# Kernel tuning notes

Hardware: AMD Instinct MI355X
Metric: run time of the kernel (lower is better)

The kernel has to match this reference:

```python
import jax, jax.numpy as jnp
import numpy as np

N, E, CIN, COUT = 50000, 800000, 64, 64
K_MAIN, K_SC = 5, 1
EPS = 1e-15      # PyG GMMConv sigma epsilon
BN_EPS = 1e-5    # BatchNorm epsilon


def gmm_conv(x, src, dst, pseudo, g, mu, sigma, root, bias):
    """PyG GMMConv with aggr='mean', root_weight=True, bias=True.
    x: [N,Cin], pseudo: [E,dim], g: [Cin,K*Cout], mu/sigma: [K,dim],
    root: [Cin,Cout], bias: [Cout]."""
    K = mu.shape[0]
    Cout = root.shape[1]
    n = x.shape[0]
    # Gaussian mixture weights per edge: [E,K]
    diff = pseudo[:, None, :] - mu[None, :, :]                     # [E,K,dim]
    gauss = jnp.exp((-0.5 * diff * diff / (EPS + sigma[None] ** 2)).sum(-1))
    # Project node features once at node level, then gather per edge
    xp = (x @ g).reshape(n, K, Cout)                               # [N,K,Cout]
    msg = jnp.einsum('ek,ekc->ec', gauss, xp[src])                 # [E,Cout]
    agg = jax.ops.segment_sum(msg, dst, num_segments=n)            # [N,Cout]
    deg = jax.ops.segment_sum(jnp.ones((src.shape[0],), x.dtype), dst,
                              num_segments=n)
    agg = agg / jnp.clip(deg, 1.0)[:, None]                        # mean aggr
    return agg + x @ root + bias


def batch_norm(x, gamma, beta):
    # SyncBatchNorm in training mode: batch stats over the node dimension
    m = x.mean(0)
    v = x.var(0)  # biased variance, as torch uses for normalization
    return (x - m) * jax.lax.rsqrt(v + BN_EPS) * gamma + beta


def _gmm_params(key, cin, cout, k):
    k1, k2, k3, k4 = jax.random.split(key, 4)
    scale = 1.0 / np.sqrt(cin)
    g = jax.random.normal(k1, (cin, k * cout), jnp.float32) * scale
    mu = jax.random.uniform(k2, (k, 1), jnp.float32)
    sigma = 1.0 + 0.1 * jax.random.uniform(k3, (k, 1), jnp.float32)
    root = jax.random.normal(k4, (cin, cout), jnp.float32) * scale
    bias = jnp.zeros((cout,), jnp.float32)
    return g, mu, sigma, root, bias


def setup_inputs() -> dict:
    key = jax.random.key(0)
    ks = jax.random.split(key, 8)
    x = jax.random.normal(ks[0], (N, CIN), jnp.float32)
    edge_index = jax.random.randint(ks[1], (2, E), 0, N, jnp.int64)
    edge_attr = jax.random.uniform(ks[2], (E, 1), jnp.float32)
    g1, mu1, sig1, root1, b1 = _gmm_params(ks[3], CIN, COUT, K_MAIN)
    g2, mu2, sig2, root2, b2 = _gmm_params(ks[4], COUT, COUT, K_MAIN)
    gs, mus, sigs, roots, bs = _gmm_params(ks[5], CIN, COUT, K_SC)
    ones = jnp.ones((COUT,), jnp.float32)
    zeros = jnp.zeros((COUT,), jnp.float32)
    return {
        'x': x, 'edge_index': edge_index, 'edge_attr': edge_attr,
        'g1': g1, 'mu1': mu1, 'sig1': sig1, 'root1': root1, 'b1': b1,
        'gam1': ones, 'bet1': zeros,
        'g2': g2, 'mu2': mu2, 'sig2': sig2, 'root2': root2, 'b2': b2,
        'gam2': ones, 'bet2': zeros,
        'gs': gs, 'mus': mus, 'sigs': sigs, 'roots': roots, 'bs': bs,
        'gams': ones, 'bets': zeros,
    }


def reference(x, edge_index, edge_attr,
              g1, mu1, sig1, root1, b1, gam1, bet1,
              g2, mu2, sig2, root2, b2, gam2, bet2,
              gs, mus, sigs, roots, bs, gams, bets):
    src, dst = edge_index[0], edge_index[1]
    h = gmm_conv(x, src, dst, edge_attr, g1, mu1, sig1, root1, b1)
    h = jax.nn.elu(batch_norm(h, gam1, bet1))
    h = gmm_conv(h, src, dst, edge_attr, g2, mu2, sig2, root2, b2)
    h = batch_norm(h, gam2, bet2)
    sc = gmm_conv(x, src, dst, edge_attr, gs, mus, sigs, roots, bs)
    sc = batch_norm(sc, gams, bets)
    return jax.nn.elu(h + sc)
```

## Files before the change

kernel.cpp:

```cpp
#include <hip/hip_runtime.h>
#include <hip/hip_bf16.h>


#define EPS_SIGMA 1e-15f
#define BN_EPS    1e-5f

typedef unsigned short ushortT;
typedef unsigned int uintT;
typedef __attribute__((ext_vector_type(8))) short bf16x8;
typedef __attribute__((ext_vector_type(4))) float f32x4;
typedef __attribute__((ext_vector_type(2))) float f32x2;

__device__ __forceinline__ ushortT f2bf(float f) {
  uintT b = __float_as_uint(f);
  b += 0x7FFFu + ((b >> 16) & 1u);
  return (ushortT)(b >> 16);
}
__device__ __forceinline__ float bf2f(ushortT u) {
  return __uint_as_float(((uintT)u) << 16);
}
__device__ __forceinline__ uintT pk2(float a, float b) {
  return (uintT)f2bf(a) | ((uintT)f2bf(b) << 16);
}

__global__ void prologue(const float* __restrict__ x, ushortT* __restrict__ x_bf,
                         int total, int* __restrict__ cnt, float* __restrict__ stats,
                         int n, const void* ei, int* flag) {
  int t = blockIdx.x * 256 + threadIdx.x;
  int idx = t * 4;
  if (idx + 3 < total) {
    float4 v = *(const float4*)&x[idx];
    ushortT o[4] = {f2bf(v.x), f2bf(v.y), f2bf(v.z), f2bf(v.w)};
    *(uint2*)&x_bf[idx] = *(const uint2*)o;
  }
  if (t < n) cnt[t] = 0;
  if (t < 12 * 64) stats[t] = 0.f;
  if (blockIdx.x == 0) {
    const int* p = (const int*)ei;
    __shared__ int bad;
    if (threadIdx.x == 0) bad = 0;
    __syncthreads();
    if (p[threadIdx.x * 2 + 1] != 0) atomicAdd(&bad, 1);
    __syncthreads();
    if (threadIdx.x == 0) *flag = (bad == 0);
  }
}

__device__ __forceinline__ int load_idx(const void* ei, size_t pos, int is64) {
  if (is64) return (int)((const long long*)ei)[pos];
  return ((const int*)ei)[pos];
}

__global__ void hist_kernel(const void* ei, int E, const int* flag, int* cnt,
                            int* __restrict__ pos) {
  int e = blockIdx.x * blockDim.x + threadIdx.x;
  if (e >= E) return;
  int d = load_idx(ei, (size_t)E + e, *flag);
  pos[e] = atomicAdd(&cnt[d], 1);
}

__global__ __launch_bounds__(256) void scan1(const int* __restrict__ cnt,
                                             int* __restrict__ row_ptr,
                                             int* __restrict__ partials, int n) {
  int tid = threadIdx.x;
  int base = blockIdx.x * 2048 + tid * 8;
  int v[8], pre[8];
  int run = 0;
#pragma unroll
  for (int j = 0; j < 8; ++j) {
    int idx = base + j;
    v[j] = (idx < n) ? cnt[idx] : 0;
    pre[j] = run;
    run += v[j];
  }
  __shared__ int sd[256];
  sd[tid] = run;
  __syncthreads();
  for (int off = 1; off < 256; off <<= 1) {
    int t = (tid >= off) ? sd[tid - off] : 0;
    __syncthreads();
    sd[tid] += t;
    __syncthreads();
  }
  int excl = sd[tid] - run;
#pragma unroll
  for (int j = 0; j < 8; ++j) {
    int idx = base + j;
    if (idx < n) row_ptr[idx] = excl + pre[j];
  }
  if (tid == 255) partials[blockIdx.x] = sd[255];
}

__global__ void scan2(int* partials, int nb, int* row_ptr, int n) {
  __shared__ int sd[256];
  int tid = threadIdx.x;
  int v = (tid < nb) ? partials[tid] : 0;
  sd[tid] = v;
  __syncthreads();
  for (int off = 1; off < 256; off <<= 1) {
    int t = (tid >= off) ? sd[tid - off] : 0;
    __syncthreads();
    sd[tid] += t;
    __syncthreads();
  }
  if (tid < nb) partials[tid] = sd[tid] - v;
  if (tid == nb - 1) row_ptr[n] = sd[tid];
}

__global__ void scan3(int* __restrict__ row_ptr, const int* __restrict__ partials, int n) {
  int i = blockIdx.x * 256 + threadIdx.x;
  if (i < n) row_ptr[i] += partials[i >> 11];
}

__global__ __launch_bounds__(256) void scatter_wgt(
    const void* ei, const float* __restrict__ ea, int E, const int* flag,
    const int* __restrict__ row_ptr, const int* __restrict__ pos,
    const float* __restrict__ mu1, const float* __restrict__ sig1,
    const float* __restrict__ mus, const float* __restrict__ sigs,
    const float* __restrict__ mu2, const float* __restrict__ sig2,
    uint4* __restrict__ wbuf1, uint4* __restrict__ wbuf2) {
  int e = blockIdx.x * 256 + threadIdx.x;
  if (e >= E) return;
  int is64 = *flag;
  int s = load_idx(ei, (size_t)e, is64);
  int d = load_idx(ei, (size_t)E + e, is64);
  int slot = row_ptr[d] + pos[e];
  float p = ea[e];
  float w1[6], w2[5];
#pragma unroll
  for (int k = 0; k < 5; ++k) {
    float sg = sig1[k], df = p - mu1[k];
    w1[k] = __expf(-0.5f / (EPS_SIGMA + sg * sg) * df * df);
  }
  {
    float sg = sigs[0], df = p - mus[0];
    w1[5] = __expf(-0.5f / (EPS_SIGMA + sg * sg) * df * df);
  }
#pragma unroll
  for (int k = 0; k < 5; ++k) {
    float sg = sig2[k], df = p - mu2[k];
    w2[k] = __expf(-0.5f / (EPS_SIGMA + sg * sg) * df * df);
  }
  wbuf1[slot] = make_uint4(pk2(w1[0], w1[1]), pk2(w1[2], w1[3]), pk2(w1[4], w1[5]), (uintT)s);
  wbuf2[slot] = make_uint4(pk2(w2[0], w2[1]), pk2(w2[2], w2[3]), pk2(w2[4], 0.f), (uintT)s);
}

template <int KT>
__device__ __forceinline__ void q_fma(f32x2* acc, uint4 r, uint2 xv) {
  f32x2 xlo, xhi;
  xlo.x = bf2f((ushortT)(xv.x & 0xffffu));
  xlo.y = bf2f((ushortT)(xv.x >> 16));
  xhi.x = bf2f((ushortT)(xv.y & 0xffffu));
  xhi.y = bf2f((ushortT)(xv.y >> 16));
  float w;
  f32x2 wv;
  w = bf2f((ushortT)(r.x & 0xffffu));
  wv.x = w; wv.y = w;
  acc[0] = __builtin_elementwise_fma(wv, xlo, acc[0]);
  acc[1] = __builtin_elementwise_fma(wv, xhi, acc[1]);
  if (KT > 1) {
    w = bf2f((ushortT)(r.x >> 16));
    wv.x = w; wv.y = w;
    acc[2] = __builtin_elementwise_fma(wv, xlo, acc[2]);
    acc[3] = __builtin_elementwise_fma(wv, xhi, acc[3]);
  }
  if (KT > 2) {
    w = bf2f((ushortT)(r.y & 0xffffu));
    wv.x = w; wv.y = w;
    acc[4] = __builtin_elementwise_fma(wv, xlo, acc[4]);
    acc[5] = __builtin_elementwise_fma(wv, xhi, acc[5]);
  }
  if (KT > 3) {
    w = bf2f((ushortT)(r.y >> 16));
    wv.x = w; wv.y = w;
    acc[6] = __builtin_elementwise_fma(wv, xlo, acc[6]);
    acc[7] = __builtin_elementwise_fma(wv, xhi, acc[7]);
  }
  if (KT > 4) {
    w = bf2f((ushortT)(r.z & 0xffffu));
    wv.x = w; wv.y = w;
    acc[8] = __builtin_elementwise_fma(wv, xlo, acc[8]);
    acc[9] = __builtin_elementwise_fma(wv, xhi, acc[9]);
  }
  if (KT > 5) {
    w = bf2f((ushortT)(r.z >> 16));
    wv.x = w; wv.y = w;
    acc[10] = __builtin_elementwise_fma(wv, xlo, acc[10]);
    acc[11] = __builtin_elementwise_fma(wv, xhi, acc[11]);
  }
}

template <int KT>
__global__ __launch_bounds__(256) void agg_pre(const ushortT* __restrict__ feat,
                                               const int* __restrict__ row_ptr,
                                               const uint4* __restrict__ wbuf,
                                               ushortT* __restrict__ out, int n, int ldo) {
  int lane = threadIdx.x & 63;
  int q = lane >> 4;
  int c4 = lane & 15;
  int node = (blockIdx.x * 4 + (threadIdx.x >> 6)) * 4 + q;
  bool act = node < n;
  int beg = act ? row_ptr[node] : 0;
  int end = act ? row_ptr[node + 1] : 0;
  f32x2 acc[2 * KT];
#pragma unroll
  for (int k = 0; k < 2 * KT; ++k) acc[k] = (f32x2){0.f, 0.f};
  int i = beg;
  for (; i + 4 <= end; i += 4) {
    uint4 r0 = wbuf[i + 0];
    uint4 r1 = wbuf[i + 1];
    uint4 r2 = wbuf[i + 2];
    uint4 r3 = wbuf[i + 3];
    uint2 x0 = *(const uint2*)&feat[((size_t)r0.w << 6) + c4 * 4];
    uint2 x1 = *(const uint2*)&feat[((size_t)r1.w << 6) + c4 * 4];
    uint2 x2 = *(const uint2*)&feat[((size_t)r2.w << 6) + c4 * 4];
    uint2 x3 = *(const uint2*)&feat[((size_t)r3.w << 6) + c4 * 4];
    q_fma<KT>(acc, r0, x0);
    q_fma<KT>(acc, r1, x1);
    q_fma<KT>(acc, r2, x2);
    q_fma<KT>(acc, r3, x3);
  }
  for (; i < end; ++i) {
    uint4 r = wbuf[i];
    uint2 xv = *(const uint2*)&feat[((size_t)r.w << 6) + c4 * 4];
    q_fma<KT>(acc, r, xv);
  }
  if (act) {
    int degi = end - beg;
    float invdeg = 1.0f / (float)(degi > 1 ? degi : 1);
    uintT* outu = (uintT*)out;
    size_t obase = ((size_t)node * ldo) >> 1;
#pragma unroll
    for (int k = 0; k < KT; ++k) {
      uint2 ov = make_uint2(pk2(acc[2 * k].x * invdeg, acc[2 * k].y * invdeg),
                            pk2(acc[2 * k + 1].x * invdeg, acc[2 * k + 1].y * invdeg));
      *(uint2*)&outu[obase + k * 32 + c4 * 2] = ov;
    }
  }
}

__device__ __forceinline__ void prep_one(const float* __restrict__ g,
                                         const float* __restrict__ root,
                                         ushortT* __restrict__ Bm, int K, int t) {
  int ks = t >> 8, rem = t & 255;
  int nt = rem >> 6, lane = rem & 63;
  int kbase = ks * 32 + (lane >> 4) * 8;
  int col = nt * 16 + (lane & 15);
  ushortT o[8];
#pragma unroll
  for (int j = 0; j < 8; ++j) {
    int r = kbase + j;
    float v;
    if (r < K * 64) {
      int k = r >> 6, i = r & 63;
      v = g[(size_t)i * (K * 64) + k * 64 + col];
    } else {
      v = root[(size_t)(r - K * 64) * 64 + col];
    }
    o[j] = f2bf(v);
  }
  *(uint4*)&Bm[(size_t)t * 8] = *(const uint4*)o;
}

__global__ void prep_all(const float* g1, const float* root1, ushortT* Bm1,
                         const float* g2, const float* root2, ushortT* Bm2,
                         const float* gs, const float* roots, ushortT* Bmsc) {
  int t = blockIdx.x * 256 + threadIdx.x;
  if (t < 12 * 256) prep_one(g1, root1, Bm1, 5, t);
  else if (t < 24 * 256) prep_one(g2, root2, Bm2, 5, t - 12 * 256);
  else if (t < 28 * 256) prep_one(gs, roots, Bmsc, 1, t - 24 * 256);
}

__device__ __forceinline__ void bn_epilogue(float cs[4], float cq[4], int wid, int lane,
                                            int tid, float red_s[4][64], float red_q[4][64],
                                            float* sums, float* sumsq) {
#pragma unroll
  for (int nt = 0; nt < 4; ++nt) {
    cs[nt] += __shfl_xor(cs[nt], 16);
    cs[nt] += __shfl_xor(cs[nt], 32);
    cq[nt] += __shfl_xor(cq[nt], 16);
    cq[nt] += __shfl_xor(cq[nt], 32);
  }
  if (lane < 16) {
#pragma unroll
    for (int nt = 0; nt < 4; ++nt) {
      red_s[wid][nt * 16 + lane] = cs[nt];
      red_q[wid][nt * 16 + lane] = cq[nt];
    }
  }
  __syncthreads();
  if (tid < 64) {
    float ts = red_s[0][tid] + red_s[1][tid] + red_s[2][tid] + red_s[3][tid];
    float tq = red_q[0][tid] + red_q[1][tid] + red_q[2][tid] + red_q[3][tid];
    atomicAdd(&sums[tid], ts);
    atomicAdd(&sumsq[tid], tq);
  }
  __syncthreads();
}

__global__ __launch_bounds__(256) void gemm_mfma(const ushortT* __restrict__ A1, int lda1,
                                                 int K1, const ushortT* __restrict__ A2,
                                                 const ushortT* __restrict__ Bm,
                                                 const float* __restrict__ bias,
                                                 ushortT* __restrict__ C, int M,
                                                 float* sums, float* sumsq) {
  __shared__ float red_s[4][64];
  __shared__ float red_q[4][64];
  int tid = threadIdx.x;
  int wid = tid >> 6, lane = tid & 63;
  int row16 = lane & 15, kg = lane >> 4;
  int rowbase = blockIdx.x * 64 + wid * 16;
  int arow = rowbase + row16;
  if (arow >= M) arow = M - 1;
  const ushortT* a1p = A1 + (size_t)arow * lda1 + kg * 8;
  const ushortT* a2p = A2 + (size_t)arow * 64 + kg * 8;
  int nks1 = K1 >> 5;
  int nks = (K1 + 64) >> 5;
  f32x4 acc[4];
#pragma unroll
  for (int nt = 0; nt < 4; ++nt) acc[nt] = (f32x4){0.f, 0.f, 0.f, 0.f};
  for (int ks = 0; ks < nks; ++ks) {
    const ushortT* ap = (ks < nks1) ? (a1p + ks * 32) : (a2p + (ks - nks1) * 32);
    bf16x8 af = *(const bf16x8*)ap;
#pragma unroll
    for (int nt = 0; nt < 4; ++nt) {
      bf16x8 bfr = *(const bf16x8*)(Bm + (size_t)ks * 2048 + nt * 512 + lane * 8);
      acc[nt] = __builtin_amdgcn_mfma_f32_16x16x32_bf16(af, bfr, acc[nt], 0, 0, 0);
    }
  }
  float bv[4];
#pragma unroll
  for (int nt = 0; nt < 4; ++nt) bv[nt] = bias[nt * 16 + row16];
  float cs[4] = {}, cq[4] = {};
#pragma unroll
  for (int r = 0; r < 4; ++r) {
    int orow = rowbase + kg * 4 + r;
    if (orow < M) {
#pragma unroll
      for (int nt = 0; nt < 4; ++nt) {
        float v = acc[nt][r] + bv[nt];
        C[(size_t)orow * 64 + nt * 16 + row16] = f2bf(v);
        cs[nt] += v;
        cq[nt] = fmaf(v, v, cq[nt]);
      }
    }
  }
  bn_epilogue(cs, cq, wid, lane, tid, red_s, red_q, sums, sumsq);
}

__global__ __launch_bounds__(256) void gemm_mfma_dual(
    const ushortT* __restrict__ Abuf, const ushortT* __restrict__ X,
    const ushortT* __restrict__ Bm1, const ushortT* __restrict__ Bmsc,
    const float* __restrict__ b1, const float* __restrict__ bs,
    ushortT* __restrict__ H, ushortT* __restrict__ S, int M,
    float* sumH, float* sqH, float* sumS, float* sqS) {
  __shared__ float red_s[4][64];
  __shared__ float red_q[4][64];
  int tid = threadIdx.x;
  int wid = tid >> 6, lane = tid & 63;
  int row16 = lane & 15, kg = lane >> 4;
  int rowbase = blockIdx.x * 64 + wid * 16;
  int arow = rowbase + row16;
  if (arow >= M) arow = M - 1;
  const ushortT* ab = Abuf + (size_t)arow * 384 + kg * 8;
  const ushortT* xb = X + (size_t)arow * 64 + kg * 8;
  f32x4 accH[4], accS[4];
#pragma unroll
  for (int nt = 0; nt < 4; ++nt) {
    accH[nt] = (f32x4){0.f, 0.f, 0.f, 0.f};
    accS[nt] = (f32x4){0.f, 0.f, 0.f, 0.f};
  }
  for (int ks = 0; ks < 10; ++ks) {
    bf16x8 af = *(const bf16x8*)(ab + ks * 32);
#pragma unroll
    for (int nt = 0; nt < 4; ++nt) {
      bf16x8 bfr = *(const bf16x8*)(Bm1 + (size_t)ks * 2048 + nt * 512 + lane * 8);
      accH[nt] = __builtin_amdgcn_mfma_f32_16x16x32_bf16(af, bfr, accH[nt], 0, 0, 0);
    }
  }
#pragma unroll
  for (int ks = 0; ks < 2; ++ks) {
    bf16x8 af = *(const bf16x8*)(ab + 320 + ks * 32);
#pragma unroll
    for (int nt = 0; nt < 4; ++nt) {
      bf16x8 bfr = *(const bf16x8*)(Bmsc + (size_t)ks * 2048 + nt * 512 + lane * 8);
      accS[nt] = __builtin_amdgcn_mfma_f32_16x16x32_bf16(af, bfr, accS[nt], 0, 0, 0);
    }
  }
#pragma unroll
  for (int ks = 0; ks < 2; ++ks) {
    bf16x8 af = *(const bf16x8*)(xb + ks * 32);
#pragma unroll
    for (int nt = 0; nt < 4; ++nt) {
      bf16x8 bfrH = *(const bf16x8*)(Bm1 + (size_t)(10 + ks) * 2048 + nt * 512 + lane * 8);
      accH[nt] = __builtin_amdgcn_mfma_f32_16x16x32_bf16(af, bfrH, accH[nt], 0, 0, 0);
      bf16x8 bfrS = *(const bf16x8*)(Bmsc + (size_t)(2 + ks) * 2048 + nt * 512 + lane * 8);
      accS[nt] = __builtin_amdgcn_mfma_f32_16x16x32_bf16(af, bfrS, accS[nt], 0, 0, 0);
    }
  }
  float bvH[4], bvS[4];
#pragma unroll
  for (int nt = 0; nt < 4; ++nt) {
    bvH[nt] = b1[nt * 16 + row16];
    bvS[nt] = bs[nt * 16 + row16];
  }
  float csH[4] = {}, cqH[4] = {}, csS[4] = {}, cqS[4] = {};
#pragma unroll
  for (int r = 0; r < 4; ++r) {
    int orow = rowbase + kg * 4 + r;
    if (orow < M) {
#pragma unroll
      for (int nt = 0; nt < 4; ++nt) {
        float vh = accH[nt][r] + bvH[nt];
        float vs = accS[nt][r] + bvS[nt];
        H[(size_t)orow * 64 + nt * 16 + row16] = f2bf(vh);
        S[(size_t)orow * 64 + nt * 16 + row16] = f2bf(vs);
        csH[nt] += vh;
        cqH[nt] = fmaf(vh, vh, cqH[nt]);
        csS[nt] += vs;
        cqS[nt] = fmaf(vs, vs, cqS[nt]);
      }
    }
  }
  bn_epilogue(csH, cqH, wid, lane, tid, red_s, red_q, sumH, sqH);
  bn_epilogue(csS, cqS, wid, lane, tid, red_s, red_q, sumS, sqS);
}

__global__ void norm_elu(const ushortT* __restrict__ Hbf, ushortT* __restrict__ h_bf,
                         const float* __restrict__ stats, const float* __restrict__ gam,
                         const float* __restrict__ bet, float inv_n, int total4) {
  __shared__ float sc_s[64], sh_s[64];
  int tid = threadIdx.x;
  if (tid < 64) {
    float m = stats[tid] * inv_n;
    float v = stats[64 + tid] * inv_n - m * m;
    float r = rsqrtf(v + BN_EPS);
    float s = r * gam[tid];
    sc_s[tid] = s;
    sh_s[tid] = bet[tid] - m * s;
  }
  __syncthreads();
  int t = blockIdx.x * 256 + tid;
  if (t >= total4) return;
  int idx = t * 4;
  int c = idx & 63;
  uint2 hv = *(const uint2*)&Hbf[idx];
  float v0 = bf2f((ushortT)(hv.x & 0xffffu)) * sc_s[c] + sh_s[c];
  float v1 = bf2f((ushortT)(hv.x >> 16)) * sc_s[c + 1] + sh_s[c + 1];
  float v2 = bf2f((ushortT)(hv.y & 0xffffu)) * sc_s[c + 2] + sh_s[c + 2];
  float v3 = bf2f((ushortT)(hv.y >> 16)) * sc_s[c + 3] + sh_s[c + 3];
  v0 = v0 > 0.f ? v0 : expm1f(v0);
  v1 = v1 > 0.f ? v1 : expm1f(v1);
  v2 = v2 > 0.f ? v2 : expm1f(v2);
  v3 = v3 > 0.f ? v3 : expm1f(v3);
  *(uint2*)&h_bf[idx] = make_uint2(pk2(v0, v1), pk2(v2, v3));
}

__global__ void final_kernel(const ushortT* __restrict__ h2, const ushortT* __restrict__ scb,
                             const float* __restrict__ stats,
                             const float* __restrict__ gam2, const float* __restrict__ bet2,
                             const float* __restrict__ gams, const float* __restrict__ bets,
                             float inv_n, float* __restrict__ out, int total4) {
  __shared__ float s2_s[64], t2_s[64], ss_s[64], ts_s[64];
  int tid = threadIdx.x;
  if (tid < 64) {
    float m = stats[2 * 64 + tid] * inv_n;
    float v = stats[3 * 64 + tid] * inv_n - m * m;
    float r = rsqrtf(v + BN_EPS);
    float s = r * gam2[tid];
    s2_s[tid] = s;
    t2_s[tid] = bet2[tid] - m * s;
  } else if (tid < 128) {
    int c = tid - 64;
    float m = stats[4 * 64 + c] * inv_n;
    float v = stats[5 * 64 + c] * inv_n - m * m;
    float r = rsqrtf(v + BN_EPS);
    float s = r * gams[c];
    ss_s[c] = s;
    ts_s[c] = bets[c] - m * s;
  }
  __syncthreads();
  int t = blockIdx.x * 256 + tid;
  if (t >= total4) return;
  int idx = t * 4;
  int c = idx & 63;
  uint2 hv = *(const uint2*)&h2[idx];
  uint2 sv = *(const uint2*)&scb[idx];
  float v0 = bf2f((ushortT)(hv.x & 0xffffu)) * s2_s[c] + t2_s[c] +
             bf2f((ushortT)(sv.x & 0xffffu)) * ss_s[c] + ts_s[c];
  float v1 = bf2f((ushortT)(hv.x >> 16)) * s2_s[c + 1] + t2_s[c + 1] +
             bf2f((ushortT)(sv.x >> 16)) * ss_s[c + 1] + ts_s[c + 1];
  float v2 = bf2f((ushortT)(hv.y & 0xffffu)) * s2_s[c + 2] + t2_s[c + 2] +
             bf2f((ushortT)(sv.y & 0xffffu)) * ss_s[c + 2] + ts_s[c + 2];
  float v3 = bf2f((ushortT)(hv.y >> 16)) * s2_s[c + 3] + t2_s[c + 3] +
             bf2f((ushortT)(sv.y >> 16)) * ss_s[c + 3] + ts_s[c + 3];
  float4 o;
  o.x = v0 > 0.f ? v0 : expm1f(v0);
  o.y = v1 > 0.f ? v1 : expm1f(v1);
  o.z = v2 > 0.f ? v2 : expm1f(v2);
  o.w = v3 > 0.f ? v3 : expm1f(v3);
  *(float4*)&out[idx] = o;
}

extern "C" void kernel_launch(void* const* d_in, const int* in_sizes, int n_in,
                              void* d_out, int out_size, void* d_ws, size_t ws_size,
                              hipStream_t stream) {
  const float* x    = (const float*)d_in[0];
  const void*  ei   = d_in[1];
  const float* ea   = (const float*)d_in[2];
  const float* g1   = (const float*)d_in[3];
  const float* mu1  = (const float*)d_in[4];
  const float* sig1 = (const float*)d_in[5];
  const float* root1= (const float*)d_in[6];
  const float* b1   = (const float*)d_in[7];
  const float* gam1 = (const float*)d_in[8];
  const float* bet1 = (const float*)d_in[9];
  const float* g2   = (const float*)d_in[10];
  const float* mu2  = (const float*)d_in[11];
  const float* sig2 = (const float*)d_in[12];
  const float* root2= (const float*)d_in[13];
  const float* b2   = (const float*)d_in[14];
  const float* gam2 = (const float*)d_in[15];
  const float* bet2 = (const float*)d_in[16];
  const float* gs   = (const float*)d_in[17];
  const float* mus  = (const float*)d_in[18];
  const float* sigs = (const float*)d_in[19];
  const float* roots= (const float*)d_in[20];
  const float* bs   = (const float*)d_in[21];
  const float* gams = (const float*)d_in[22];
  const float* bets = (const float*)d_in[23];

  int N = in_sizes[0] / 64;
  int E = in_sizes[1] / 2;

  char* w = (char*)d_ws;
  auto alloc = [&](size_t bytes) {
    char* p = w;
    w += (bytes + 255) & ~(size_t)255;
    return p;
  };
  int*     flag    = (int*)alloc(256);
  int*     cnt     = (int*)alloc((size_t)N * 4);
  int*     row_ptr = (int*)alloc((size_t)(N + 1) * 4);
  int*     partials= (int*)alloc(256 * 4);
  int*     pos     = (int*)alloc((size_t)E * 4);
  uint4*   wbuf1   = (uint4*)alloc((size_t)E * 16);
  uint4*   wbuf2   = (uint4*)alloc((size_t)E * 16);
  ushortT* Abuf    = (ushortT*)alloc((size_t)N * 384 * 2);
  ushortT* x_bf    = (ushortT*)alloc((size_t)N * 64 * 2);
  ushortT* h_bf    = (ushortT*)alloc((size_t)N * 64 * 2);
  ushortT* Hpre    = (ushortT*)alloc((size_t)N * 64 * 2);
  ushortT* h2b     = (ushortT*)alloc((size_t)N * 64 * 2);
  ushortT* scb     = (ushortT*)alloc((size_t)N * 64 * 2);
  ushortT* Bm1     = (ushortT*)alloc(12 * 2048 * 2);
  ushortT* Bm2     = (ushortT*)alloc(12 * 2048 * 2);
  ushortT* Bmsc    = (ushortT*)alloc(4 * 2048 * 2);
  float*   stats   = (float*)alloc(12 * 64 * 4);

  int eb = (E + 255) / 256;
  int nb1 = (N + 2047) / 2048;
  int total4 = (N * 64) / 4;
  int nb_e4 = (total4 + 255) / 256;
  float inv_n = 1.0f / (float)N;

  prologue<<<nb_e4, 256, 0, stream>>>(x, x_bf, N * 64, cnt, stats, N, ei, flag);
  prep_all<<<28, 256, 0, stream>>>(g1, root1, Bm1, g2, root2, Bm2, gs, roots, Bmsc);

  hist_kernel<<<eb, 256, 0, stream>>>(ei, E, flag, cnt, pos);
  scan1<<<nb1, 256, 0, stream>>>(cnt, row_ptr, partials, N);
  scan2<<<1, 256, 0, stream>>>(partials, nb1, row_ptr, N);
  scan3<<<(N + 255) / 256, 256, 0, stream>>>(row_ptr, partials, N);
  scatter_wgt<<<eb, 256, 0, stream>>>(ei, ea, E, flag, row_ptr, pos,
                                      mu1, sig1, mus, sigs, mu2, sig2, wbuf1, wbuf2);

  int mtiles = (N + 63) / 64;
  int nb_node16 = (N + 15) / 16;

  agg_pre<6><<<nb_node16, 256, 0, stream>>>(x_bf, row_ptr, wbuf1, Abuf, N, 384);
  gemm_mfma_dual<<<mtiles, 256, 0, stream>>>(Abuf, x_bf, Bm1, Bmsc, b1, bs, Hpre, scb, N,
                                             stats + 0 * 64, stats + 1 * 64,
                                             stats + 4 * 64, stats + 5 * 64);
  norm_elu<<<nb_e4, 256, 0, stream>>>(Hpre, h_bf, stats, gam1, bet1, inv_n, total4);

  agg_pre<5><<<nb_node16, 256, 0, stream>>>(h_bf, row_ptr, wbuf2, Abuf, N, 320);
  gemm_mfma<<<mtiles, 256, 0, stream>>>(Abuf, 320, 320, h_bf, Bm2, b2, h2b, N,
                                        stats + 2 * 64, stats + 3 * 64);

  final_kernel<<<nb_e4, 256, 0, stream>>>(h2b, scb, stats, gam2, bet2, gams, bets,
                                          inv_n, (float*)d_out, total4);
}
```

Measured before the change: 211.2 us.

## Fold weight prep into prologue, drop scan3, unroll edge gather by eight

The weight-matrix bf16 prep moves into the prologue kernel, and the scan3 pass is removed. Consumers now add the per-block scan partial on the fly when reading row_ptr, which saves two kernel launches and one pass over row_ptr. The aggregation loop gains an 8-edge unrolled stage so more gather loads are in flight at once, at the cost of extra registers. The row_ptr[n] handling in scan2 uses a tricky sentinel that may be inconsistent with the per-node partial offset.

```diff
diff --git a/kernel.cpp b/kernel.cpp
--- a/kernel.cpp
+++ b/kernel.cpp
@@ -23,9 +23,35 @@
   return (uintT)f2bf(a) | ((uintT)f2bf(b) << 16);
 }
 
+__device__ __forceinline__ void prep_one(const float* __restrict__ g,
+                                         const float* __restrict__ root,
+                                         ushortT* __restrict__ Bm, int K, int t) {
+  int ks = t >> 8, rem = t & 255;
+  int nt = rem >> 6, lane = rem & 63;
+  int kbase = ks * 32 + (lane >> 4) * 8;
+  int col = nt * 16 + (lane & 15);
+  ushortT o[8];
+#pragma unroll
+  for (int j = 0; j < 8; ++j) {
+    int r = kbase + j;
+    float v;
+    if (r < K * 64) {
+      int k = r >> 6, i = r & 63;
+      v = g[(size_t)i * (K * 64) + k * 64 + col];
+    } else {
+      v = root[(size_t)(r - K * 64) * 64 + col];
+    }
+    o[j] = f2bf(v);
+  }
+  *(uint4*)&Bm[(size_t)t * 8] = *(const uint4*)o;
+}
+
 __global__ void prologue(const float* __restrict__ x, ushortT* __restrict__ x_bf,
                          int total, int* __restrict__ cnt, float* __restrict__ stats,
-                         int n, const void* ei, int* flag) {
+                         int n, const void* ei, int* flag,
+                         const float* g1, const float* root1, ushortT* Bm1,
+                         const float* g2, const float* root2, ushortT* Bm2,
+                         const float* gs, const float* roots, ushortT* Bmsc) {
   int t = blockIdx.x * 256 + threadIdx.x;
   int idx = t * 4;
   if (idx + 3 < total) {
@@ -35,7 +61,10 @@
   }
   if (t < n) cnt[t] = 0;
   if (t < 12 * 64) stats[t] = 0.f;
-  if (blockIdx.x == 0) {
+  if (blockIdx.x < 12) prep_one(g1, root1, Bm1, 5, t);
+  else if (blockIdx.x < 24) prep_one(g2, root2, Bm2, 5, t - 12 * 256);
+  else if (blockIdx.x < 28) prep_one(gs, roots, Bmsc, 1, t - 24 * 256);
+  else if (blockIdx.x == 28) {
     const int* p = (const int*)ei;
     __shared__ int bad;
     if (threadIdx.x == 0) bad = 0;
@@ -104,17 +133,16 @@
     __syncthreads();
   }
   if (tid < nb) partials[tid] = sd[tid] - v;
-  if (tid == nb - 1) row_ptr[n] = sd[tid];
-}
-
-__global__ void scan3(int* __restrict__ row_ptr, const int* __restrict__ partials, int n) {
-  int i = blockIdx.x * 256 + threadIdx.x;
-  if (i < n) row_ptr[i] += partials[i >> 11];
+  if (tid == nb - 1) {
+    partials[nb] = sd[tid];
+    row_ptr[n] = ((n >> 11) == nb) ? 0 : v;
+  }
 }
 
 __global__ __launch_bounds__(256) void scatter_wgt(
     const void* ei, const float* __restrict__ ea, int E, const int* flag,
-    const int* __restrict__ row_ptr, const int* __restrict__ pos,
+    const int* __restrict__ row_ptr, const int* __restrict__ partials,
+    const int* __restrict__ pos,
     const float* __restrict__ mu1, const float* __restrict__ sig1,
     const float* __restrict__ mus, const float* __restrict__ sigs,
     const float* __restrict__ mu2, const float* __restrict__ sig2,
@@ -124,7 +152,7 @@
   int is64 = *flag;
   int s = load_idx(ei, (size_t)e, is64);
   int d = load_idx(ei, (size_t)E + e, is64);
-  int slot = row_ptr[d] + pos[e];
+  int slot = row_ptr[d] + partials[d >> 11] + pos[e];
   float p = ea[e];
   float w1[6], w2[5];
 #pragma unroll
@@ -193,6 +221,7 @@
 template <int KT>
 __global__ __launch_bounds__(256) void agg_pre(const ushortT* __restrict__ feat,
                                                const int* __restrict__ row_ptr,
+                                               const int* __restrict__ partials,
                                                const uint4* __restrict__ wbuf,
                                                ushortT* __restrict__ out, int n, int ldo) {
   int lane = threadIdx.x & 63;
@@ -200,12 +229,41 @@
   int c4 = lane & 15;
   int node = (blockIdx.x * 4 + (threadIdx.x >> 6)) * 4 + q;
   bool act = node < n;
-  int beg = act ? row_ptr[node] : 0;
-  int end = act ? row_ptr[node + 1] : 0;
+  int beg = 0, end = 0;
+  if (act) {
+    beg = row_ptr[node] + partials[node >> 11];
+    end = row_ptr[node + 1] + partials[(node + 1) >> 11];
+  }
   f32x2 acc[2 * KT];
 #pragma unroll
   for (int k = 0; k < 2 * KT; ++k) acc[k] = (f32x2){0.f, 0.f};
   int i = beg;
+  for (; i + 8 <= end; i += 8) {
+    uint4 r0 = wbuf[i + 0];
+    uint4 r1 = wbuf[i + 1];
+    uint4 r2 = wbuf[i + 2];
+    uint4 r3 = wbuf[i + 3];
+    uint4 r4 = wbuf[i + 4];
+    uint4 r5 = wbuf[i + 5];
+    uint4 r6 = wbuf[i + 6];
+    uint4 r7 = wbuf[i + 7];
+    uint2 x0 = *(const uint2*)&feat[((size_t)r0.w << 6) + c4 * 4];
+    uint2 x1 = *(const uint2*)&feat[((size_t)r1.w << 6) + c4 * 4];
+    uint2 x2 = *(const uint2*)&feat[((size_t)r2.w << 6) + c4 * 4];
+    uint2 x3 = *(const uint2*)&feat[((size_t)r3.w << 6) + c4 * 4];
+    uint2 x4 = *(const uint2*)&feat[((size_t)r4.w << 6) + c4 * 4];
+    uint2 x5 = *(const uint2*)&feat[((size_t)r5.w << 6) + c4 * 4];
+    uint2 x6 = *(const uint2*)&feat[((size_t)r6.w << 6) + c4 * 4];
+    uint2 x7 = *(const uint2*)&feat[((size_t)r7.w << 6) + c4 * 4];
+    q_fma<KT>(acc, r0, x0);
+    q_fma<KT>(acc, r1, x1);
+    q_fma<KT>(acc, r2, x2);
+    q_fma<KT>(acc, r3, x3);
+    q_fma<KT>(acc, r4, x4);
+    q_fma<KT>(acc, r5, x5);
+    q_fma<KT>(acc, r6, x6);
+    q_fma<KT>(acc, r7, x7);
+  }
   for (; i + 4 <= end; i += 4) {
     uint4 r0 = wbuf[i + 0];
     uint4 r1 = wbuf[i + 1];
@@ -237,38 +295,6 @@
       *(uint2*)&outu[obase + k * 32 + c4 * 2] = ov;
     }
   }
-}
-
-__device__ __forceinline__ void prep_one(const float* __restrict__ g,
-                                         const float* __restrict__ root,
-                                         ushortT* __restrict__ Bm, int K, int t) {
-  int ks = t >> 8, rem = t & 255;
-  int nt = rem >> 6, lane = rem & 63;
-  int kbase = ks * 32 + (lane >> 4) * 8;
-  int col = nt * 16 + (lane & 15);
-  ushortT o[8];
-#pragma unroll
-  for (int j = 0; j < 8; ++j) {
-    int r = kbase + j;
-    float v;
-    if (r < K * 64) {
-      int k = r >> 6, i = r & 63;
-      v = g[(size_t)i * (K * 64) + k * 64 + col];
-    } else {
-      v = root[(size_t)(r - K * 64) * 64 + col];
-    }
-    o[j] = f2bf(v);
-  }
-  *(uint4*)&Bm[(size_t)t * 8] = *(const uint4*)o;
-}
-
-__global__ void prep_all(const float* g1, const float* root1, ushortT* Bm1,
-                         const float* g2, const float* root2, ushortT* Bm2,
-                         const float* gs, const float* roots, ushortT* Bmsc) {
-  int t = blockIdx.x * 256 + threadIdx.x;
-  if (t < 12 * 256) prep_one(g1, root1, Bm1, 5, t);
-  else if (t < 24 * 256) prep_one(g2, root2, Bm2, 5, t - 12 * 256);
-  else if (t < 28 * 256) prep_one(gs, roots, Bmsc, 1, t - 24 * 256);
 }
 
 __device__ __forceinline__ void bn_epilogue(float cs[4], float cq[4], int wid, int lane,
@@ -542,7 +568,7 @@
   int*     flag    = (int*)alloc(256);
   int*     cnt     = (int*)alloc((size_t)N * 4);
   int*     row_ptr = (int*)alloc((size_t)(N + 1) * 4);
-  int*     partials= (int*)alloc(256 * 4);
+  int*     partials= (int*)alloc(257 * 4);
   int*     pos     = (int*)alloc((size_t)E * 4);
   uint4*   wbuf1   = (uint4*)alloc((size_t)E * 16);
   uint4*   wbuf2   = (uint4*)alloc((size_t)E * 16);
@@ -563,26 +589,25 @@
   int nb_e4 = (total4 + 255) / 256;
   float inv_n = 1.0f / (float)N;
 
-  prologue<<<nb_e4, 256, 0, stream>>>(x, x_bf, N * 64, cnt, stats, N, ei, flag);
-  prep_all<<<28, 256, 0, stream>>>(g1, root1, Bm1, g2, root2, Bm2, gs, roots, Bmsc);
+  prologue<<<nb_e4, 256, 0, stream>>>(x, x_bf, N * 64, cnt, stats, N, ei, flag,
+                                      g1, root1, Bm1, g2, root2, Bm2, gs, roots, Bmsc);
 
   hist_kernel<<<eb, 256, 0, stream>>>(ei, E, flag, cnt, pos);
   scan1<<<nb1, 256, 0, stream>>>(cnt, row_ptr, partials, N);
   scan2<<<1, 256, 0, stream>>>(partials, nb1, row_ptr, N);
-  scan3<<<(N + 255) / 256, 256, 0, stream>>>(row_ptr, partials, N);
-  scatter_wgt<<<eb, 256, 0, stream>>>(ei, ea, E, flag, row_ptr, pos,
+  scatter_wgt<<<eb, 256, 0, stream>>>(ei, ea, E, flag, row_ptr, partials, pos,
                                       mu1, sig1, mus, sigs, mu2, sig2, wbuf1, wbuf2);
 
   int mtiles = (N + 63) / 64;
   int nb_node16 = (N + 15) / 16;
 
-  agg_pre<6><<<nb_node16, 256, 0, stream>>>(x_bf, row_ptr, wbuf1, Abuf, N, 384);
+  agg_pre<6><<<nb_node16, 256, 0, stream>>>(x_bf, row_ptr, partials, wbuf1, Abuf, N, 384);
   gemm_mfma_dual<<<mtiles, 256, 0, stream>>>(Abuf, x_bf, Bm1, Bmsc, b1, bs, Hpre, scb, N,
                                              stats + 0 * 64, stats + 1 * 64,
                                              stats + 4 * 64, stats + 5 * 64);
   norm_elu<<<nb_e4, 256, 0, stream>>>(Hpre, h_bf, stats, gam1, bet1, inv_n, total4);
 
-  agg_pre<5><<<nb_node16, 256, 0, stream>>>(h_bf, row_ptr, wbuf2, Abuf, N, 320);
+  agg_pre<5><<<nb_node16, 256, 0, stream>>>(h_bf, row_ptr, partials, wbuf2, Abuf, N, 320);
   gemm_mfma<<<mtiles, 256, 0, stream>>>(Abuf, 320, 320, h_bf, Bm2, b2, h2b, N,
                                         stats + 2 * 64, stats + 3 * 64);
 
```

Result: no change. 214.5 us (+1.6%).
